# Optimization experiments

Hardware: AMD Instinct MI355X
Metric: run time of the kernel (lower is better)

Reference implementation:

```python
import jax, jax.numpy as jnp
import numpy as np

EMBED_DIM = 1024
NUM_HEADS = 16
DEPTH = EMBED_DIM // NUM_HEADS  # 64
B, S = 4, 2048


def setup_inputs() -> dict:
    key = jax.random.key(0)
    ks = jax.random.split(key, 12)
    sc = 0.02
    return {
        "q": jax.random.normal(ks[0], (B, S, EMBED_DIM), jnp.float32),
        "k": jax.random.normal(ks[1], (B, S, EMBED_DIM), jnp.float32),
        "v": jax.random.normal(ks[2], (B, S, EMBED_DIM), jnp.float32),
        # per-head Dense(depth) weights stacked over heads: [H, D, depth]
        "wq": jax.random.normal(ks[3], (NUM_HEADS, EMBED_DIM, DEPTH), jnp.float32) * sc,
        "bq": jnp.zeros((NUM_HEADS, DEPTH), jnp.float32),
        "wk": jax.random.normal(ks[4], (NUM_HEADS, EMBED_DIM, DEPTH), jnp.float32) * sc,
        "bk": jnp.zeros((NUM_HEADS, DEPTH), jnp.float32),
        "wv": jax.random.normal(ks[5], (NUM_HEADS, EMBED_DIM, DEPTH), jnp.float32) * sc,
        "bv": jnp.zeros((NUM_HEADS, DEPTH), jnp.float32),
        # final Dense(embedding_dim): [D, D]
        "wo": jax.random.normal(ks[6], (EMBED_DIM, EMBED_DIM), jnp.float32) * sc,
        "bo": jnp.zeros((EMBED_DIM,), jnp.float32),
        "use_mask": 1,
    }


def reference(q, k, v, wq, bq, wk, bk, wv, bv, wo, bo, use_mask):
    # Batched per-head projections (equivalent to H separate Dense layers).
    qh = jnp.einsum('bsd,hde->bhse', q, wq) + bq[None, :, None, :]
    kh = jnp.einsum('bsd,hde->bhse', k, wk) + bk[None, :, None, :]
    vh = jnp.einsum('bsd,hde->bhse', v, wv) + bv[None, :, None, :]

    scale = 1.0 / jnp.sqrt(jnp.asarray(DEPTH, jnp.float32))
    logits = jnp.einsum('bhqe,bhke->bhqk', qh, kh) * scale  # [B,H,Sq,Sk]
    if use_mask:
        Sq, Sk = qh.shape[2], kh.shape[2]
        causal = jnp.triu(jnp.ones((Sq, Sk), jnp.float32), k=1)
        logits = logits + causal[None, None, :, :] * (-1e9)
    attn = jax.nn.softmax(logits, axis=-1)
    out_h = jnp.einsum('bhqk,bhke->bhqe', attn, vh)  # [B,H,Sq,depth]
    # concat heads along last dim -> [B,Sq,H*depth]
    bsz, H, Sq, dep = out_h.shape
    concat = out_h.transpose(0, 2, 1, 3).reshape(bsz, Sq, H * dep)
    return concat @ wo + bo
```

## Files before the change

kernel.cpp:

```cpp
#include <hip/hip_runtime.h>

#define B_ 4
#define S_ 2048
#define H_ 16
#define D_ 64
#define E_ 1024
#define M_ 8192

typedef __attribute__((ext_vector_type(8))) __bf16 bf16x8;
typedef __attribute__((ext_vector_type(4))) __bf16 bf16x4;
typedef __attribute__((ext_vector_type(4))) float f32x4;
typedef __attribute__((ext_vector_type(16))) float f32x16;

__device__ __forceinline__ void gload_lds16(const void* g, void* l) {
  __builtin_amdgcn_global_load_lds(
      (const __attribute__((address_space(1))) unsigned int*)g,
      (__attribute__((address_space(3))) unsigned int*)l, 16, 0, 0);
}

__device__ __forceinline__ unsigned pk2(float a, float b) {
  union { __bf16 h; unsigned short u; } ua, ub;
  ua.h = (__bf16)a; ub.h = (__bf16)b;
  return ((unsigned)ub.u << 16) | (unsigned)ua.u;
}

__global__ void prep_all(const float* __restrict__ q, const float* __restrict__ k,
                         const float* __restrict__ v, const float* __restrict__ wq,
                         const float* __restrict__ wk, const float* __restrict__ wv,
                         const float* __restrict__ wo, __bf16* __restrict__ Aq,
                         __bf16* __restrict__ Ak, __bf16* __restrict__ Av,
                         __bf16* __restrict__ Bq, __bf16* __restrict__ Bk,
                         __bf16* __restrict__ Bv, __bf16* __restrict__ Bo) {
  const int y = blockIdx.y;
  if (y < 3) {
    const float* src = (y == 0) ? q : (y == 1) ? k : v;
    __bf16* dst = (y == 0) ? Aq : (y == 1) ? Ak : Av;
    const int i = blockIdx.x * blockDim.x + threadIdx.x;
    const float4 vv = ((const float4*)src)[i];
    bf16x4 o;
    o.x = (__bf16)vv.x; o.y = (__bf16)vv.y; o.z = (__bf16)vv.z; o.w = (__bf16)vv.w;
    ((bf16x4*)dst)[i] = o;
  } else {
    if (blockIdx.x >= 4096) return;
    const int yy = y - 3;
    const int idx = blockIdx.x * 256 + threadIdx.x;
    const int n = idx >> 10, kk = idx & 1023;
    if (yy < 3) {
      const float* w = (yy == 0) ? wq : (yy == 1) ? wk : wv;
      __bf16* out = (yy == 0) ? Bq : (yy == 1) ? Bk : Bv;
      out[idx] = (__bf16)w[((size_t)(n >> 6) << 16) + (kk << 6) + (n & 63)];
    } else {
      Bo[idx] = (__bf16)wo[((size_t)kk << 10) + n];
    }
  }
}

__global__ __launch_bounds__(256) void gemm_qk(
    const __bf16* __restrict__ Aq, const __bf16* __restrict__ Ak,
    const __bf16* __restrict__ Bq, const __bf16* __restrict__ Bk,
    const float* __restrict__ bq, const float* __restrict__ bk,
    __bf16* __restrict__ qhb, __bf16* __restrict__ khb) {
  constexpr int K = 1024;
  __shared__ __bf16 As[128 * 64];
  __shared__ __bf16 Bs[128 * 64];
  const int t = threadIdx.x;
  const int w = t >> 6, l = t & 63;
  const int isK = blockIdx.y >> 3;
  const __bf16* A = isK ? Ak : Aq;
  const __bf16* Bt = isK ? Bk : Bq;
  const float* bias = isK ? bk : bq;
  __bf16* C = isK ? khb : qhb;
  const int m0 = blockIdx.x * 128, n0 = (blockIdx.y & 7) * 128;
  f32x4 acc[4][4] = {};

  for (int kt = 0; kt < K / 64; ++kt) {
    const int kb = kt * 64;
#pragma unroll
    for (int j = 0; j < 4; ++j) {
      const int ci = (j * 4 + w) * 64 + l;
      const int row = ci >> 3;
      const int c = (ci & 7) ^ (row & 7);
      gload_lds16(A + (size_t)(m0 + row) * K + kb + c * 8, As + (j * 4 + w) * 512);
      gload_lds16(Bt + (size_t)(n0 + row) * K + kb + c * 8, Bs + (j * 4 + w) * 512);
    }
    __syncthreads();
#pragma unroll
    for (int kk = 0; kk < 64; kk += 32) {
      bf16x8 af[4], bfr[4];
#pragma unroll
      for (int f = 0; f < 4; ++f) {
        const int ra = (w >> 1) * 64 + f * 16 + (l & 15);
        const int ca = ((kk >> 3) + (l >> 4)) ^ (ra & 7);
        af[f] = *(const bf16x8*)(As + ra * 64 + ca * 8);
        const int rb = (w & 1) * 64 + f * 16 + (l & 15);
        const int cb = ((kk >> 3) + (l >> 4)) ^ (rb & 7);
        bfr[f] = *(const bf16x8*)(Bs + rb * 64 + cb * 8);
      }
#pragma unroll
      for (int mf = 0; mf < 4; ++mf)
#pragma unroll
        for (int nf = 0; nf < 4; ++nf)
          acc[mf][nf] = __builtin_amdgcn_mfma_f32_16x16x32_bf16(af[mf], bfr[nf],
                                                                acc[mf][nf], 0, 0, 0);
    }
    __syncthreads();
  }

#pragma unroll
  for (int mf = 0; mf < 4; ++mf)
#pragma unroll
    for (int nf = 0; nf < 4; ++nf)
#pragma unroll
      for (int r = 0; r < 4; ++r) {
        const int gm = m0 + (w >> 1) * 64 + mf * 16 + (l >> 4) * 4 + r;
        const int gn = n0 + (w & 1) * 64 + nf * 16 + (l & 15);
        const float val = acc[mf][nf][r] + bias[gn];
        C[(((size_t)(gm >> 11) * H_ + (gn >> 6)) * S_ + (gm & 2047)) * D_ + (gn & 63)] =
            (__bf16)val;
      }
}

template <int MODE>
__global__ __launch_bounds__(256) void gemm_bt(const __bf16* __restrict__ A,
                                               const __bf16* __restrict__ Bt,
                                               const float* __restrict__ bias,
                                               void* __restrict__ Cout) {
  constexpr int K = 1024;
  __shared__ __bf16 As[128 * 64];
  __shared__ __bf16 Bs[128 * 64];
  const int t = threadIdx.x;
  const int w = t >> 6, l = t & 63;
  const int m0 = blockIdx.x * 128, n0 = blockIdx.y * 128;
  f32x4 acc[4][4] = {};

  for (int kt = 0; kt < K / 64; ++kt) {
    const int kb = kt * 64;
#pragma unroll
    for (int j = 0; j < 4; ++j) {
      const int ci = (j * 4 + w) * 64 + l;
      const int row = ci >> 3;
      const int c = (ci & 7) ^ (row & 7);
      gload_lds16(A + (size_t)(m0 + row) * K + kb + c * 8, As + (j * 4 + w) * 512);
      gload_lds16(Bt + (size_t)(n0 + row) * K + kb + c * 8, Bs + (j * 4 + w) * 512);
    }
    __syncthreads();
#pragma unroll
    for (int kk = 0; kk < 64; kk += 32) {
      bf16x8 af[4], bfr[4];
#pragma unroll
      for (int f = 0; f < 4; ++f) {
        const int ra = (w >> 1) * 64 + f * 16 + (l & 15);
        const int ca = ((kk >> 3) + (l >> 4)) ^ (ra & 7);
        af[f] = *(const bf16x8*)(As + ra * 64 + ca * 8);
        const int rb = (w & 1) * 64 + f * 16 + (l & 15);
        const int cb = ((kk >> 3) + (l >> 4)) ^ (rb & 7);
        bfr[f] = *(const bf16x8*)(Bs + rb * 64 + cb * 8);
      }
#pragma unroll
      for (int mf = 0; mf < 4; ++mf)
#pragma unroll
        for (int nf = 0; nf < 4; ++nf)
          acc[mf][nf] = __builtin_amdgcn_mfma_f32_16x16x32_bf16(af[mf], bfr[nf],
                                                                acc[mf][nf], 0, 0, 0);
    }
    __syncthreads();
  }

#pragma unroll
  for (int mf = 0; mf < 4; ++mf) {
#pragma unroll
    for (int nf = 0; nf < 4; ++nf) {
#pragma unroll
      for (int r = 0; r < 4; ++r) {
        const int gm = m0 + (w >> 1) * 64 + mf * 16 + (l >> 4) * 4 + r;
        const int gn = n0 + (w & 1) * 64 + nf * 16 + (l & 15);
        const float val = acc[mf][nf][r] + ((MODE == 1) ? bias[gm] : bias[gn]);
        if constexpr (MODE == 1) {
          ((__bf16*)Cout)[(((size_t)(gn >> 11) * H_ + (gm >> 6)) * D_ + (gm & 63)) * S_ + (gn & 2047)] =
              (__bf16)val;
        } else {
          ((float*)Cout)[(size_t)gm * 1024 + gn] = val;
        }
      }
    }
  }
}

__device__ __forceinline__ void stage_k128(const __bf16* __restrict__ Kb, int kt,
                                           __bf16* Kdst, int t, int w) {
#pragma unroll
  for (int j = 0; j < 4; ++j) {
    const int ci = j * 256 + t;
    const int row = ci >> 3;
    const int sc = (ci & 7) ^ (row & 7);
    gload_lds16(Kb + (size_t)(kt * 128 + row) * D_ + sc * 8, Kdst + j * 2048 + w * 512);
  }
}
__device__ __forceinline__ void stage_v64(const __bf16* __restrict__ Vb, int col0,
                                          __bf16* Vdst, int t, int w) {
#pragma unroll
  for (int j = 0; j < 2; ++j) {
    const int ci = j * 256 + t;
    const int row = ci >> 3;
    const int sc = (ci & 7) ^ (row & 7);
    gload_lds16(Vb + (size_t)row * S_ + col0 + sc * 8, Vdst + j * 2048 + w * 512);
  }
}

__global__ __launch_bounds__(256, 2) void attn_fused(const __bf16* __restrict__ qh,
                                                     const __bf16* __restrict__ kh,
                                                     const __bf16* __restrict__ vT,
                                                     __bf16* __restrict__ concat,
                                                     const int* __restrict__ use_mask_p) {
  __shared__ __bf16 Ks[2][128 * 64];
  __shared__ __bf16 Vs[2][2][64 * 64];
  const int t = threadIdx.x, w = t >> 6, l = t & 63;
  const int lo = l & 31, hi = l >> 5;
  const int bh = blockIdx.x, pr = blockIdx.y;
  const int usemask = *use_mask_p;
  const __bf16* Qb = qh + (size_t)bh * S_ * D_;
  const __bf16* Kb = kh + (size_t)bh * S_ * D_;
  const __bf16* Vb = vT + (size_t)bh * D_ * S_;
  const int b = bh >> 4, hh = bh & 15;
  constexpr float CEXP = 0.125f * 1.4426950408889634f;

  bf16x8 ones;
#pragma unroll
  for (int i = 0; i < 8; ++i) ones[i] = (__bf16)1.0f;

  int cur = 0;
  for (int half = 0; half < 2; ++half) {
    const int qt = half ? (15 - pr) : pr;
    const int qrow0 = qt * 128 + w * 32;
    const int nkt = usemask ? (qt + 1) : (S_ / 128);
    const int ktw = usemask ? (2 * qt + (w >> 1)) : (1 << 30);

    bf16x8 qf[4];
#pragma unroll
    for (int ks = 0; ks < 4; ++ks)
      qf[ks] = *(const bf16x8*)(Qb + (size_t)(qrow0 + lo) * D_ + ks * 16 + hi * 8);

    float m = -3e38f;
    f32x16 lsacc = {};
    f32x16 o0 = {}, o1 = {};

    stage_k128(Kb, 0, &Ks[cur][0], t, w);
    stage_v64(Vb, 0, &Vs[cur][0][0], t, w);
    stage_v64(Vb, 64, &Vs[cur][1][0], t, w);

    for (int kt = 0; kt < nkt; ++kt) {
      __builtin_amdgcn_sched_barrier(0);
      asm volatile("s_waitcnt vmcnt(0)" ::: "memory");
      __builtin_amdgcn_s_barrier();
      __builtin_amdgcn_sched_barrier(0);

      if (kt + 1 < nkt) {
        const int nxt = cur ^ 1;
        stage_k128(Kb, kt + 1, &Ks[nxt][0], t, w);
        stage_v64(Vb, (kt + 1) * 128, &Vs[nxt][0][0], t, w);
        stage_v64(Vb, (kt + 1) * 128 + 64, &Vs[nxt][1][0], t, w);
      }

#pragma unroll
      for (int sub = 0; sub < 2; ++sub) {
        const int st = 2 * kt + sub;
        if (st <= ktw) {
          const __bf16* Ksub = &Ks[cur][sub * 64 * 64];
          const __bf16* Vsub = &Vs[cur][sub][0];

          f32x16 s0 = {}, s1 = {};
          __builtin_amdgcn_s_setprio(1);
#pragma unroll
          for (int ks = 0; ks < 4; ++ks) {
            const int ch = ((ks << 1) | hi) ^ (lo & 7);
            const bf16x8 k0 = *(const bf16x8*)(Ksub + lo * 64 + ch * 8);
            const bf16x8 k1 = *(const bf16x8*)(Ksub + (32 + lo) * 64 + ch * 8);
            s0 = __builtin_amdgcn_mfma_f32_32x32x16_bf16(k0, qf[ks], s0, 0, 0, 0);
            s1 = __builtin_amdgcn_mfma_f32_32x32x16_bf16(k1, qf[ks], s1, 0, 0, 0);
          }
          __builtin_amdgcn_s_setprio(0);

          if (usemask && st == ktw) {
            const int qloc = ((w & 1) << 5) + lo;
#pragma unroll
            for (int r = 0; r < 16; ++r) {
              const int kv0 = (r & 3) + 8 * (r >> 2) + 4 * hi;
              if (kv0 > qloc) s0[r] = -1e30f;
              if (kv0 + 32 > qloc) s1[r] = -1e30f;
            }
          }

          float pm = s0[0];
#pragma unroll
          for (int r = 1; r < 16; ++r) pm = fmaxf(pm, s0[r]);
#pragma unroll
          for (int r = 0; r < 16; ++r) pm = fmaxf(pm, s1[r]);

          if (!__all(pm - m <= 64.0f)) {
            const float pmp = fmaxf(pm, __shfl_xor(pm, 32));
            const float mn = fmaxf(m, pmp);
            const float al = __builtin_amdgcn_exp2f((m - mn) * CEXP);
            m = mn;
            lsacc[0] *= al;
            o0 *= al;
            o1 *= al;
          }
          const float mneg = -m * CEXP;

          unsigned W0[4][2], W1[4][2];
#pragma unroll
          for (int j = 0; j < 4; ++j) {
            float p0 = __builtin_amdgcn_exp2f(__builtin_fmaf(s0[4 * j + 0], CEXP, mneg));
            float p1 = __builtin_amdgcn_exp2f(__builtin_fmaf(s0[4 * j + 1], CEXP, mneg));
            float p2 = __builtin_amdgcn_exp2f(__builtin_fmaf(s0[4 * j + 2], CEXP, mneg));
            float p3 = __builtin_amdgcn_exp2f(__builtin_fmaf(s0[4 * j + 3], CEXP, mneg));
            W0[j][0] = pk2(p0, p1);
            W0[j][1] = pk2(p2, p3);
            float q0 = __builtin_amdgcn_exp2f(__builtin_fmaf(s1[4 * j + 0], CEXP, mneg));
            float q1 = __builtin_amdgcn_exp2f(__builtin_fmaf(s1[4 * j + 1], CEXP, mneg));
            float q2 = __builtin_amdgcn_exp2f(__builtin_fmaf(s1[4 * j + 2], CEXP, mneg));
            float q3 = __builtin_amdgcn_exp2f(__builtin_fmaf(s1[4 * j + 3], CEXP, mneg));
            W1[j][0] = pk2(q0, q1);
            W1[j][1] = pk2(q2, q3);
          }

          bf16x8 pa[4];
#pragma unroll
          for (int ks = 0; ks < 4; ++ks) {
            const int c = ks & 1;
            unsigned x0, x1, y0, y1;
            if ((ks >> 1) == 0) {
              x0 = W0[2 * c][0]; x1 = W0[2 * c][1];
              y0 = W0[2 * c + 1][0]; y1 = W0[2 * c + 1][1];
            } else {
              x0 = W1[2 * c][0]; x1 = W1[2 * c][1];
              y0 = W1[2 * c + 1][0]; y1 = W1[2 * c + 1][1];
            }
            asm volatile("v_permlane32_swap_b32 %0, %1" : "+v"(x0), "+v"(y0));
            asm volatile("v_permlane32_swap_b32 %0, %1" : "+v"(x1), "+v"(y1));
            union { unsigned u[4]; bf16x8 v; } uu;
            uu.u[0] = x0; uu.u[1] = x1; uu.u[2] = y0; uu.u[3] = y1;
            pa[ks] = uu.v;
          }

          __builtin_amdgcn_s_setprio(1);
#pragma unroll
          for (int ks = 0; ks < 4; ++ks) {
            const int ch = ((ks << 1) | hi) ^ (lo & 7);
            const bf16x8 v0 = *(const bf16x8*)(Vsub + lo * 64 + ch * 8);
            const bf16x8 v1 = *(const bf16x8*)(Vsub + (32 + lo) * 64 + ch * 8);
            o0 = __builtin_amdgcn_mfma_f32_32x32x16_bf16(v0, pa[ks], o0, 0, 0, 0);
            o1 = __builtin_amdgcn_mfma_f32_32x32x16_bf16(v1, pa[ks], o1, 0, 0, 0);
            lsacc = __builtin_amdgcn_mfma_f32_32x32x16_bf16(ones, pa[ks], lsacc, 0, 0, 0);
          }
          __builtin_amdgcn_s_setprio(0);
        }
      }
      cur ^= 1;
    }

    const float inv = 1.0f / lsacc[0];
    const size_t rowbase = ((size_t)(b * S_ + qrow0 + lo)) * E_ + hh * 64;
#pragma unroll
    for (int rr = 0; rr < 4; ++rr) {
      bf16x4 v0, v1;
#pragma unroll
      for (int bb = 0; bb < 4; ++bb) {
        v0[bb] = (__bf16)(o0[4 * rr + bb] * inv);
        v1[bb] = (__bf16)(o1[4 * rr + bb] * inv);
      }
      *(bf16x4*)(concat + rowbase + 8 * rr + 4 * hi) = v0;
      *(bf16x4*)(concat + rowbase + 32 + 8 * rr + 4 * hi) = v1;
    }
  }
}

extern "C" void kernel_launch(void* const* d_in, const int* in_sizes, int n_in,
                              void* d_out, int out_size, void* d_ws, size_t ws_size,
                              hipStream_t stream) {
  const float* q = (const float*)d_in[0];
  const float* k = (const float*)d_in[1];
  const float* v = (const float*)d_in[2];
  const float* wq = (const float*)d_in[3];
  const float* bq = (const float*)d_in[4];
  const float* wk = (const float*)d_in[5];
  const float* bk = (const float*)d_in[6];
  const float* wv = (const float*)d_in[7];
  const float* bv = (const float*)d_in[8];
  const float* wo = (const float*)d_in[9];
  const float* bo = (const float*)d_in[10];
  const int* use_mask = (const int*)d_in[11];
  (void)in_sizes; (void)n_in; (void)out_size; (void)ws_size;

  char* ws = (char*)d_ws;
  __bf16* Aq = (__bf16*)ws;
  __bf16* Ak = Aq + (size_t)M_ * E_;
  __bf16* Av = Ak + (size_t)M_ * E_;
  __bf16* Bq = Av + (size_t)M_ * E_;
  __bf16* Bk = Bq + (size_t)E_ * E_;
  __bf16* Bv = Bk + (size_t)E_ * E_;
  __bf16* Bo = Bv + (size_t)E_ * E_;
  __bf16* qhb = Bo + (size_t)E_ * E_;
  __bf16* khb = qhb + (size_t)8388608;
  __bf16* vTb = khb + (size_t)8388608;
  __bf16* concat = Aq;

  prep_all<<<dim3(8192, 7), 256, 0, stream>>>(q, k, v, wq, wk, wv, wo,
                                              Aq, Ak, Av, Bq, Bk, Bv, Bo);
  gemm_qk<<<dim3(64, 16), 256, 0, stream>>>(Aq, Ak, Bq, Bk, bq, bk, qhb, khb);
  gemm_bt<1><<<dim3(8, 64), 256, 0, stream>>>(Bv, Av, bv, vTb);
  attn_fused<<<dim3(64, 8), 256, 0, stream>>>(qhb, khb, vTb, concat, use_mask);
  gemm_bt<2><<<dim3(64, 8), 256, 0, stream>>>(concat, Bo, bo, d_out);
}
```

Baseline: 194.3 us.

## Process both causal query tiles in one KV sweep to share K/V staging

New measurement: 194.4 us (median of 2 runs). Within noise of the previous version (+0.1%).

```diff
diff --git a/kernel.cpp b/kernel.cpp
--- a/kernel.cpp
+++ b/kernel.cpp
@@ -11,6 +11,8 @@
 typedef __attribute__((ext_vector_type(4))) __bf16 bf16x4;
 typedef __attribute__((ext_vector_type(4))) float f32x4;
 typedef __attribute__((ext_vector_type(16))) float f32x16;
+
+#define CEXPF (0.125f * 1.4426950408889634f)
 
 __device__ __forceinline__ void gload_lds16(const void* g, void* l) {
   __builtin_amdgcn_global_load_lds(
@@ -207,6 +209,99 @@
   }
 }
 
+__device__ __forceinline__ void attn_subtile(const __bf16* __restrict__ Ksub,
+                                             const __bf16* __restrict__ Vsub,
+                                             const bf16x8* qf, const bf16x8 ones,
+                                             int lo, int hi, int qloc, bool diag,
+                                             float& m, f32x16& lsacc,
+                                             f32x16& o0, f32x16& o1) {
+  f32x16 s0 = {}, s1 = {};
+  __builtin_amdgcn_s_setprio(1);
+#pragma unroll
+  for (int ks = 0; ks < 4; ++ks) {
+    const int ch = ((ks << 1) | hi) ^ (lo & 7);
+    const bf16x8 k0 = *(const bf16x8*)(Ksub + lo * 64 + ch * 8);
+    const bf16x8 k1 = *(const bf16x8*)(Ksub + (32 + lo) * 64 + ch * 8);
+    s0 = __builtin_amdgcn_mfma_f32_32x32x16_bf16(k0, qf[ks], s0, 0, 0, 0);
+    s1 = __builtin_amdgcn_mfma_f32_32x32x16_bf16(k1, qf[ks], s1, 0, 0, 0);
+  }
+  __builtin_amdgcn_s_setprio(0);
+
+  if (diag) {
+#pragma unroll
+    for (int r = 0; r < 16; ++r) {
+      const int kv0 = (r & 3) + 8 * (r >> 2) + 4 * hi;
+      if (kv0 > qloc) s0[r] = -1e30f;
+      if (kv0 + 32 > qloc) s1[r] = -1e30f;
+    }
+  }
+
+  float pm = s0[0];
+#pragma unroll
+  for (int r = 1; r < 16; ++r) pm = fmaxf(pm, s0[r]);
+#pragma unroll
+  for (int r = 0; r < 16; ++r) pm = fmaxf(pm, s1[r]);
+
+  if (!__all(pm - m <= 64.0f)) {
+    const float pmp = fmaxf(pm, __shfl_xor(pm, 32));
+    const float mn = fmaxf(m, pmp);
+    const float al = __builtin_amdgcn_exp2f((m - mn) * CEXPF);
+    m = mn;
+    lsacc[0] *= al;
+    o0 *= al;
+    o1 *= al;
+  }
+  const float mneg = -m * CEXPF;
+
+  unsigned W0[4][2], W1[4][2];
+#pragma unroll
+  for (int j = 0; j < 4; ++j) {
+    float p0 = __builtin_amdgcn_exp2f(__builtin_fmaf(s0[4 * j + 0], CEXPF, mneg));
+    float p1 = __builtin_amdgcn_exp2f(__builtin_fmaf(s0[4 * j + 1], CEXPF, mneg));
+    float p2 = __builtin_amdgcn_exp2f(__builtin_fmaf(s0[4 * j + 2], CEXPF, mneg));
+    float p3 = __builtin_amdgcn_exp2f(__builtin_fmaf(s0[4 * j + 3], CEXPF, mneg));
+    W0[j][0] = pk2(p0, p1);
+    W0[j][1] = pk2(p2, p3);
+    float q0 = __builtin_amdgcn_exp2f(__builtin_fmaf(s1[4 * j + 0], CEXPF, mneg));
+    float q1 = __builtin_amdgcn_exp2f(__builtin_fmaf(s1[4 * j + 1], CEXPF, mneg));
+    float q2 = __builtin_amdgcn_exp2f(__builtin_fmaf(s1[4 * j + 2], CEXPF, mneg));
+    float q3 = __builtin_amdgcn_exp2f(__builtin_fmaf(s1[4 * j + 3], CEXPF, mneg));
+    W1[j][0] = pk2(q0, q1);
+    W1[j][1] = pk2(q2, q3);
+  }
+
+  bf16x8 pa[4];
+#pragma unroll
+  for (int ks = 0; ks < 4; ++ks) {
+    const int c = ks & 1;
+    unsigned x0, x1, y0, y1;
+    if ((ks >> 1) == 0) {
+      x0 = W0[2 * c][0]; x1 = W0[2 * c][1];
+      y0 = W0[2 * c + 1][0]; y1 = W0[2 * c + 1][1];
+    } else {
+      x0 = W1[2 * c][0]; x1 = W1[2 * c][1];
+      y0 = W1[2 * c + 1][0]; y1 = W1[2 * c + 1][1];
+    }
+    asm volatile("v_permlane32_swap_b32 %0, %1" : "+v"(x0), "+v"(y0));
+    asm volatile("v_permlane32_swap_b32 %0, %1" : "+v"(x1), "+v"(y1));
+    union { unsigned u[4]; bf16x8 v; } uu;
+    uu.u[0] = x0; uu.u[1] = x1; uu.u[2] = y0; uu.u[3] = y1;
+    pa[ks] = uu.v;
+  }
+
+  __builtin_amdgcn_s_setprio(1);
+#pragma unroll
+  for (int ks = 0; ks < 4; ++ks) {
+    const int ch = ((ks << 1) | hi) ^ (lo & 7);
+    const bf16x8 v0 = *(const bf16x8*)(Vsub + lo * 64 + ch * 8);
+    const bf16x8 v1 = *(const bf16x8*)(Vsub + (32 + lo) * 64 + ch * 8);
+    o0 = __builtin_amdgcn_mfma_f32_32x32x16_bf16(v0, pa[ks], o0, 0, 0, 0);
+    o1 = __builtin_amdgcn_mfma_f32_32x32x16_bf16(v1, pa[ks], o1, 0, 0, 0);
+    lsacc = __builtin_amdgcn_mfma_f32_32x32x16_bf16(ones, pa[ks], lsacc, 0, 0, 0);
+  }
+  __builtin_amdgcn_s_setprio(0);
+}
+
 __global__ __launch_bounds__(256, 2) void attn_fused(const __bf16* __restrict__ qh,
                                                      const __bf16* __restrict__ kh,
                                                      const __bf16* __restrict__ vT,
@@ -222,155 +317,80 @@
   const __bf16* Kb = kh + (size_t)bh * S_ * D_;
   const __bf16* Vb = vT + (size_t)bh * D_ * S_;
   const int b = bh >> 4, hh = bh & 15;
-  constexpr float CEXP = 0.125f * 1.4426950408889634f;
+  const int qloc = ((w & 1) << 5) + lo;
 
   bf16x8 ones;
 #pragma unroll
   for (int i = 0; i < 8; ++i) ones[i] = (__bf16)1.0f;
 
+  const int qtA = pr, qtB = 15 - pr;
+  const int qrow0A = qtA * 128 + w * 32, qrow0B = qtB * 128 + w * 32;
+  const int nkt = usemask ? (qtB + 1) : (S_ / 128);
+  const int ktwA = usemask ? (2 * qtA + (w >> 1)) : (1 << 30);
+  const int ktwB = usemask ? (2 * qtB + (w >> 1)) : (1 << 30);
+
+  bf16x8 qfA[4], qfB[4];
+#pragma unroll
+  for (int ks = 0; ks < 4; ++ks) {
+    qfA[ks] = *(const bf16x8*)(Qb + (size_t)(qrow0A + lo) * D_ + ks * 16 + hi * 8);
+    qfB[ks] = *(const bf16x8*)(Qb + (size_t)(qrow0B + lo) * D_ + ks * 16 + hi * 8);
+  }
+
+  float mA = -3e38f, mB = -3e38f;
+  f32x16 lsA = {}, lsB = {};
+  f32x16 oA0 = {}, oA1 = {}, oB0 = {}, oB1 = {};
+
   int cur = 0;
-  for (int half = 0; half < 2; ++half) {
-    const int qt = half ? (15 - pr) : pr;
-    const int qrow0 = qt * 128 + w * 32;
-    const int nkt = usemask ? (qt + 1) : (S_ / 128);
-    const int ktw = usemask ? (2 * qt + (w >> 1)) : (1 << 30);
-
-    bf16x8 qf[4];
-#pragma unroll
-    for (int ks = 0; ks < 4; ++ks)
-      qf[ks] = *(const bf16x8*)(Qb + (size_t)(qrow0 + lo) * D_ + ks * 16 + hi * 8);
-
-    float m = -3e38f;
-    f32x16 lsacc = {};
-    f32x16 o0 = {}, o1 = {};
-
-    stage_k128(Kb, 0, &Ks[cur][0], t, w);
-    stage_v64(Vb, 0, &Vs[cur][0][0], t, w);
-    stage_v64(Vb, 64, &Vs[cur][1][0], t, w);
-
-    for (int kt = 0; kt < nkt; ++kt) {
-      __builtin_amdgcn_sched_barrier(0);
-      asm volatile("s_waitcnt vmcnt(0)" ::: "memory");
-      __builtin_amdgcn_s_barrier();
-      __builtin_amdgcn_sched_barrier(0);
-
-      if (kt + 1 < nkt) {
-        const int nxt = cur ^ 1;
-        stage_k128(Kb, kt + 1, &Ks[nxt][0], t, w);
-        stage_v64(Vb, (kt + 1) * 128, &Vs[nxt][0][0], t, w);
-        stage_v64(Vb, (kt + 1) * 128 + 64, &Vs[nxt][1][0], t, w);
+  stage_k128(Kb, 0, &Ks[0][0], t, w);
+  stage_v64(Vb, 0, &Vs[0][0][0], t, w);
+  stage_v64(Vb, 64, &Vs[0][1][0], t, w);
+
+  for (int kt = 0; kt < nkt; ++kt) {
+    __builtin_amdgcn_sched_barrier(0);
+    asm volatile("s_waitcnt vmcnt(0)" ::: "memory");
+    __builtin_amdgcn_s_barrier();
+    __builtin_amdgcn_sched_barrier(0);
+
+    if (kt + 1 < nkt) {
+      const int nxt = cur ^ 1;
+      stage_k128(Kb, kt + 1, &Ks[nxt][0], t, w);
+      stage_v64(Vb, (kt + 1) * 128, &Vs[nxt][0][0], t, w);
+      stage_v64(Vb, (kt + 1) * 128 + 64, &Vs[nxt][1][0], t, w);
+    }
+
+#pragma unroll
+    for (int sub = 0; sub < 2; ++sub) {
+      const int st = 2 * kt + sub;
+      const __bf16* Ksub = &Ks[cur][sub * 64 * 64];
+      const __bf16* Vsub = &Vs[cur][sub][0];
+      if (st <= ktwA)
+        attn_subtile(Ksub, Vsub, qfA, ones, lo, hi, qloc,
+                     usemask && st == ktwA, mA, lsA, oA0, oA1);
+      if (st <= ktwB)
+        attn_subtile(Ksub, Vsub, qfB, ones, lo, hi, qloc,
+                     usemask && st == ktwB, mB, lsB, oB0, oB1);
+    }
+    cur ^= 1;
+  }
+
+  {
+    const float invA = 1.0f / lsA[0], invB = 1.0f / lsB[0];
+    const size_t rbA = ((size_t)(b * S_ + qrow0A + lo)) * E_ + hh * 64;
+    const size_t rbB = ((size_t)(b * S_ + qrow0B + lo)) * E_ + hh * 64;
+#pragma unroll
+    for (int rr = 0; rr < 4; ++rr) {
+      bf16x4 a0, a1, b0, b1;
+#pragma unroll
+      for (int bb = 0; bb < 4; ++bb) {
+        a0[bb] = (__bf16)(oA0[4 * rr + bb] * invA);
+        a1[bb] = (__bf16)(oA1[4 * rr + bb] * invA);
+        b0[bb] = (__bf16)(oB0[4 * rr + bb] * invB);
+        b1[bb] = (__bf16)(oB1[4 * rr + bb] * invB);
       }
-
-#pragma unroll
-      for (int sub = 0; sub < 2; ++sub) {
-        const int st = 2 * kt + sub;
-        if (st <= ktw) {
-          const __bf16* Ksub = &Ks[cur][sub * 64 * 64];
-          const __bf16* Vsub = &Vs[cur][sub][0];
-
-          f32x16 s0 = {}, s1 = {};
-          __builtin_amdgcn_s_setprio(1);
-#pragma unroll
-          for (int ks = 0; ks < 4; ++ks) {
-            const int ch = ((ks << 1) | hi) ^ (lo & 7);
-            const bf16x8 k0 = *(const bf16x8*)(Ksub + lo * 64 + ch * 8);
-            const bf16x8 k1 = *(const bf16x8*)(Ksub + (32 + lo) * 64 + ch * 8);
-            s0 = __builtin_amdgcn_mfma_f32_32x32x16_bf16(k0, qf[ks], s0, 0, 0, 0);
-            s1 = __builtin_amdgcn_mfma_f32_32x32x16_bf16(k1, qf[ks], s1, 0, 0, 0);
-          }
-          __builtin_amdgcn_s_setprio(0);
-
-          if (usemask && st == ktw) {
-            const int qloc = ((w & 1) << 5) + lo;
-#pragma unroll
-            for (int r = 0; r < 16; ++r) {
-              const int kv0 = (r & 3) + 8 * (r >> 2) + 4 * hi;
-              if (kv0 > qloc) s0[r] = -1e30f;
-              if (kv0 + 32 > qloc) s1[r] = -1e30f;
-            }
-          }
-
-          float pm = s0[0];
-#pragma unroll
-          for (int r = 1; r < 16; ++r) pm = fmaxf(pm, s0[r]);
-#pragma unroll
-          for (int r = 0; r < 16; ++r) pm = fmaxf(pm, s1[r]);
-
-          if (!__all(pm - m <= 64.0f)) {
-            const float pmp = fmaxf(pm, __shfl_xor(pm, 32));
-            const float mn = fmaxf(m, pmp);
-            const float al = __builtin_amdgcn_exp2f((m - mn) * CEXP);
-            m = mn;
-            lsacc[0] *= al;
-            o0 *= al;
-            o1 *= al;
-          }
-          const float mneg = -m * CEXP;
-
-          unsigned W0[4][2], W1[4][2];
-#pragma unroll
-          for (int j = 0; j < 4; ++j) {
-            float p0 = __builtin_amdgcn_exp2f(__builtin_fmaf(s0[4 * j + 0], CEXP, mneg));
-            float p1 = __builtin_amdgcn_exp2f(__builtin_fmaf(s0[4 * j + 1], CEXP, mneg));
-            float p2 = __builtin_amdgcn_exp2f(__builtin_fmaf(s0[4 * j + 2], CEXP, mneg));
-            float p3 = __builtin_amdgcn_exp2f(__builtin_fmaf(s0[4 * j + 3], CEXP, mneg));
-            W0[j][0] = pk2(p0, p1);
-            W0[j][1] = pk2(p2, p3);
-            float q0 = __builtin_amdgcn_exp2f(__builtin_fmaf(s1[4 * j + 0], CEXP, mneg));
-            float q1 = __builtin_amdgcn_exp2f(__builtin_fmaf(s1[4 * j + 1], CEXP, mneg));
-            float q2 = __builtin_amdgcn_exp2f(__builtin_fmaf(s1[4 * j + 2], CEXP, mneg));
-            float q3 = __builtin_amdgcn_exp2f(__builtin_fmaf(s1[4 * j + 3], CEXP, mneg));
-            W1[j][0] = pk2(q0, q1);
-            W1[j][1] = pk2(q2, q3);
-          }
-
-          bf16x8 pa[4];
-#pragma unroll
-          for (int ks = 0; ks < 4; ++ks) {
-            const int c = ks & 1;
-            unsigned x0, x1, y0, y1;
-            if ((ks >> 1) == 0) {
-              x0 = W0[2 * c][0]; x1 = W0[2 * c][1];
-              y0 = W0[2 * c + 1][0]; y1 = W0[2 * c + 1][1];
-            } else {
-              x0 = W1[2 * c][0]; x1 = W1[2 * c][1];
-              y0 = W1[2 * c + 1][0]; y1 = W1[2 * c + 1][1];
-            }
-            asm volatile("v_permlane32_swap_b32 %0, %1" : "+v"(x0), "+v"(y0));
-            asm volatile("v_permlane32_swap_b32 %0, %1" : "+v"(x1), "+v"(y1));
-            union { unsigned u[4]; bf16x8 v; } uu;
-            uu.u[0] = x0; uu.u[1] = x1; uu.u[2] = y0; uu.u[3] = y1;
-            pa[ks] = uu.v;
-          }
-
-          __builtin_amdgcn_s_setprio(1);
-#pragma unroll
-          for (int ks = 0; ks < 4; ++ks) {
-            const int ch = ((ks << 1) | hi) ^ (lo & 7);
-            const bf16x8 v0 = *(const bf16x8*)(Vsub + lo * 64 + ch * 8);
-            const bf16x8 v1 = *(const bf16x8*)(Vsub + (32 + lo) * 64 + ch * 8);
-            o0 = __builtin_amdgcn_mfma_f32_32x32x16_bf16(v0, pa[ks], o0, 0, 0, 0);
-            o1 = __builtin_amdgcn_mfma_f32_32x32x16_bf16(v1, pa[ks], o1, 0, 0, 0);
-            lsacc = __builtin_amdgcn_mfma_f32_32x32x16_bf16(ones, pa[ks], lsacc, 0, 0, 0);
-          }
-          __builtin_amdgcn_s_setprio(0);
-        }
-      }
-      cur ^= 1;
-    }
-
-    const float inv = 1.0f / lsacc[0];
-    const size_t rowbase = ((size_t)(b * S_ + qrow0 + lo)) * E_ + hh * 64;
-#pragma unroll
-    for (int rr = 0; rr < 4; ++rr) {
-      bf16x4 v0, v1;
-#pragma unroll
-      for (int bb = 0; bb < 4; ++bb) {
-        v0[bb] = (__bf16)(o0[4 * rr + bb] * inv);
-        v1[bb] = (__bf16)(o1[4 * rr + bb] * inv);
-      }
-      *(bf16x4*)(concat + rowbase + 8 * rr + 4 * hi) = v0;
-      *(bf16x4*)(concat + rowbase + 32 + 8 * rr + 4 * hi) = v1;
+      *(bf16x4*)(concat + rbA + 8 * rr + 4 * hi) = a0;
+      *(bf16x4*)(concat + rbA + 32 + 8 * rr + 4 * hi) = a1;
+      *(bf16x4*)(concat + rbB + 8 * rr + 4 * hi) = b0;
+      *(bf16x4*)(concat + rbB + 32 + 8 * rr + 4 * hi) = b1;
     }
   }
 }
```
